# Optimization experiments

Hardware: AMD Instinct MI355X
Metric: run time of the kernel (lower is better)

Reference implementation:

```python
import jax, jax.numpy as jnp
import numpy as np

N, IN_DIM, OUT_DIM, HEADS = 8192, 256, 128, 2


def setup_inputs() -> dict:
    key = jax.random.key(0)
    k1, k2, k3, k4, k5 = jax.random.split(key, 5)
    features = jax.random.normal(k1, (N, IN_DIM), dtype=jnp.float32)
    adjacency = jax.random.randint(k2, (N, N), 0, 2, dtype=jnp.int32)
    # nn.Linear(input_dim, output_dim*heads, bias=False): weight [out, in]
    W = jax.random.normal(k3, (OUT_DIM * HEADS, IN_DIM), dtype=jnp.float32) * 0.05
    attn_src = jax.random.normal(k4, (HEADS, OUT_DIM), dtype=jnp.float32) * 0.05
    attn_dst = jax.random.normal(k5, (HEADS, OUT_DIM), dtype=jnp.float32) * 0.05
    return {"features": features, "adjacency": adjacency, "W": W,
            "attn_src": attn_src, "attn_dst": attn_dst}


def reference(features, adjacency, W, attn_src, attn_dst):
    n = features.shape[0]
    # transformed: [N, H, F]
    transformed = (features @ W.T).reshape(n, HEADS, OUT_DIM)
    src_scores = jnp.einsum('nhf,hf->nh', transformed, attn_src)  # [N, H]
    dst_scores = jnp.einsum('nhf,hf->nh', transformed, attn_dst)  # [N, H]
    # logits: [N_src, N_dst, H]
    logits = jax.nn.leaky_relu(src_scores[:, None, :] + dst_scores[None, :, :],
                               negative_slope=0.2)
    mask = adjacency > 0  # [N, N]
    logits = jnp.where(mask[:, :, None], logits, -jnp.inf)
    attention = jax.nn.softmax(logits, axis=1)  # softmax over dst dim (dim=1)
    attention = jnp.nan_to_num(attention, nan=0.0, posinf=0.0, neginf=0.0)
    aggregated = jnp.einsum('ijh,jhf->ihf', attention, transformed)  # [N, H, F]
    return aggregated.mean(axis=1)  # [N, F]
```

## Files before the change

kernel.cpp:

```cpp
#include <hip/hip_runtime.h>
#include <stdint.h>
#include <stddef.h>

#define NN 8192
#define KD 256
#define CD 256
#define FD 128
#define BI 32
#define BJ 64

typedef __attribute__((ext_vector_type(4))) float f32x4;
typedef __attribute__((ext_vector_type(8))) short b16x8;

__device__ __forceinline__ unsigned short f2bf(float x) {
    unsigned int u = __float_as_uint(x);
    u += 0x7fffu + ((u >> 16) & 1u);
    return (unsigned short)(u >> 16);
}

__device__ __forceinline__ void async16(const void* g, void* l) {
    __builtin_amdgcn_global_load_lds(
        (const __attribute__((address_space(1))) unsigned int*)g,
        (__attribute__((address_space(3))) unsigned int*)l, 16, 0, 0);
}

__global__ __launch_bounds__(256) void k_transform(
    const float* __restrict__ feat, const float* __restrict__ W,
    const float* __restrict__ asrc, const float* __restrict__ adst,
    unsigned short* __restrict__ Tt, float* __restrict__ s, float* __restrict__ d)
{
    __shared__ unsigned short a_lds[64 * 32];
    __shared__ unsigned short b_lds[256 * 32];
    __shared__ unsigned short tr_lds[256 * 72];
    __shared__ float sc_lds[4][64];
    __shared__ float dc_lds[4][64];

    const int t = threadIdx.x;
    const int wave = t >> 6, lane = t & 63;
    const int l15 = lane & 15, quad = lane >> 4;
    const int n0 = blockIdx.x * 64;
    const int ai = t >> 2, ag = t & 3;

    f32x4 acc[4][4] = {};
    for (int kc = 0; kc < 8; ++kc) {
        const int k0 = kc * 32;
        __syncthreads();
        {
            const float* src = feat + (size_t)(n0 + ai) * KD + k0 + ag * 8;
            const float4 v0 = *(const float4*)src;
            const float4 v1 = *(const float4*)(src + 4);
            union { unsigned short us[8]; b16x8 v; } pk;
            pk.us[0] = f2bf(v0.x); pk.us[1] = f2bf(v0.y);
            pk.us[2] = f2bf(v0.z); pk.us[3] = f2bf(v0.w);
            pk.us[4] = f2bf(v1.x); pk.us[5] = f2bf(v1.y);
            pk.us[6] = f2bf(v1.z); pk.us[7] = f2bf(v1.w);
            const int slot = ag ^ ((ai >> 1) & 3);
            *(b16x8*)&a_lds[ai * 32 + slot * 8] = pk.v;
        }
        for (int p = 0; p < 4; ++p) {
            const int G = p * 256 + t;
            const int c = G >> 2, g = G & 3;
            const float* src = W + (size_t)c * KD + k0 + g * 8;
            const float4 v0 = *(const float4*)src;
            const float4 v1 = *(const float4*)(src + 4);
            union { unsigned short us[8]; b16x8 v; } pk;
            pk.us[0] = f2bf(v0.x); pk.us[1] = f2bf(v0.y);
            pk.us[2] = f2bf(v0.z); pk.us[3] = f2bf(v0.w);
            pk.us[4] = f2bf(v1.x); pk.us[5] = f2bf(v1.y);
            pk.us[6] = f2bf(v1.z); pk.us[7] = f2bf(v1.w);
            const int slot = g ^ ((c >> 1) & 3);
            *(b16x8*)&b_lds[c * 32 + slot * 8] = pk.v;
        }
        __syncthreads();
        b16x8 af[4], bfr[4];
        for (int mt = 0; mt < 4; ++mt) {
            const int m = mt * 16 + l15;
            af[mt] = *(const b16x8*)&a_lds[m * 32 + (quad ^ ((m >> 1) & 3)) * 8];
        }
        for (int nt = 0; nt < 4; ++nt) {
            const int c = wave * 64 + nt * 16 + l15;
            bfr[nt] = *(const b16x8*)&b_lds[c * 32 + (quad ^ ((c >> 1) & 3)) * 8];
        }
        for (int mt = 0; mt < 4; ++mt)
            for (int nt = 0; nt < 4; ++nt)
                acc[mt][nt] = __builtin_amdgcn_mfma_f32_16x16x32_bf16(
                    af[mt], bfr[nt], acc[mt][nt], 0, 0, 0);
    }

    float aS[4], aD[4];
    for (int nt = 0; nt < 4; ++nt) {
        const int c = wave * 64 + nt * 16 + l15;
        aS[nt] = asrc[c]; aD[nt] = adst[c];
    }
    for (int mt = 0; mt < 4; ++mt)
        for (int r = 0; r < 4; ++r) {
            float vs = 0.f, vd = 0.f;
            for (int nt = 0; nt < 4; ++nt) {
                const float x = acc[mt][nt][r];
                vs += x * aS[nt]; vd += x * aD[nt];
            }
            vs += __shfl_xor(vs, 1); vd += __shfl_xor(vd, 1);
            vs += __shfl_xor(vs, 2); vd += __shfl_xor(vd, 2);
            vs += __shfl_xor(vs, 4); vd += __shfl_xor(vd, 4);
            vs += __shfl_xor(vs, 8); vd += __shfl_xor(vd, 8);
            if (l15 == 0) {
                const int nl = mt * 16 + quad * 4 + r;
                sc_lds[wave][nl] = vs; dc_lds[wave][nl] = vd;
            }
        }
    for (int mt = 0; mt < 4; ++mt)
        for (int nt = 0; nt < 4; ++nt)
            for (int r = 0; r < 4; ++r) {
                const int c = wave * 64 + nt * 16 + l15;
                const int n = mt * 16 + quad * 4 + r;
                tr_lds[c * 72 + n] = f2bf(acc[mt][nt][r]);
            }
    __syncthreads();
    if (t < 128) {
        const int n = t >> 1, h = t & 1;
        s[(size_t)(n0 + n) * 2 + h] = sc_lds[h * 2][n] + sc_lds[h * 2 + 1][n];
        d[(size_t)(n0 + n) * 2 + h] = dc_lds[h * 2][n] + dc_lds[h * 2 + 1][n];
    }
    for (int p = 0; p < 8; ++p) {
        const int idx = p * 256 + t;
        const int c = idx >> 3, g = idx & 7;
        *(b16x8*)(Tt + (size_t)c * NN + n0 + g * 8) = *(const b16x8*)&tr_lds[c * 72 + g * 8];
    }
}

__global__ __launch_bounds__(256, 4) void k_gat(
    const int* __restrict__ adj, const unsigned short* __restrict__ Tt,
    const float* __restrict__ s, const float* __restrict__ d,
    float* __restrict__ num_part,
    float* __restrict__ den_part,
    int jchunk)
{
    __shared__ unsigned short tt_lds[CD * BJ];
    __shared__ unsigned short w_lds[2 * BI * BJ];

    const int t = threadIdx.x;
    const int wave = t >> 6, lane = t & 63;
    const int l15 = lane & 15, quad = lane >> 4;
    const int i0 = blockIdx.x * BI;
    const int chunk = blockIdx.y;
    const int jbase = chunk * jchunk;

    const int wi = t >> 3;
    const int j8 = t & 7;
    const int gi = i0 + wi;
    const float s0 = s[(size_t)gi * 2 + 0];
    const float s1 = s[(size_t)gi * 2 + 1];

    const int h = wave >> 1;
    const int fh = wave & 1;
    const int cbase = h * 128 + fh * 64;

    f32x4 acc[2][4] = {};
    float den0 = 0.f, den1 = 0.f;
    const int njt = jchunk / BJ;

    for (int jt = 0; jt < njt; ++jt) {
        const int j0 = jbase + jt * BJ;
        __syncthreads();
        const int* arow = adj + (size_t)gi * NN + j0 + j8 * 8;
        const int4 a0 = *(const int4*)arow;
        const int4 a1 = *(const int4*)(arow + 4);
        const float4* dvp = (const float4*)(d + (size_t)(j0 + j8 * 8) * 2);
        union { float4 v[4]; float f[16]; } dv;
        dv.v[0] = dvp[0]; dv.v[1] = dvp[1]; dv.v[2] = dvp[2]; dv.v[3] = dvp[3];
        for (int p = 0; p < 8; ++p) {
            const int G = (p * 4 + wave) * 64 + lane;
            const int c = G >> 3, gt = G & 7;
            const int g = gt ^ (c & 7);
            async16(Tt + (size_t)c * NN + j0 + g * 8,
                    (char*)tt_lds + (size_t)(p * 4 + wave) * 1024);
        }
        const int am[8] = {a0.x, a0.y, a0.z, a0.w, a1.x, a1.y, a1.z, a1.w};
        union { unsigned short us[8]; b16x8 v; } w0, w1;
        float dp0 = 0.f, dp1 = 0.f;
        for (int e = 0; e < 8; ++e) {
            float x0 = s0 + dv.f[e * 2 + 0];  x0 = x0 > 0.f ? x0 : 0.2f * x0;
            float x1 = s1 + dv.f[e * 2 + 1];  x1 = x1 > 0.f ? x1 : 0.2f * x1;
            const float e0 = am[e] != 0 ? __expf(x0) : 0.f;
            const float e1 = am[e] != 0 ? __expf(x1) : 0.f;
            dp0 += e0; dp1 += e1;
            w0.us[e] = f2bf(e0); w1.us[e] = f2bf(e1);
        }
        den0 += dp0; den1 += dp1;
        const int slot = (j8 ^ (wi & 7)) << 3;
        *(b16x8*)&w_lds[(0 * BI + wi) * BJ + slot] = w0.v;
        *(b16x8*)&w_lds[(1 * BI + wi) * BJ + slot] = w1.v;
        __syncthreads();
        for (int ks = 0; ks < 2; ++ks) {
            const int gidx = ks * 4 + quad;
            b16x8 af[2], bfr[4];
            for (int mt = 0; mt < 2; ++mt) {
                const int m = mt * 16 + l15;
                af[mt] = *(const b16x8*)&w_lds[(h * BI + m) * BJ + ((gidx ^ (m & 7)) << 3)];
            }
            for (int nt = 0; nt < 4; ++nt) {
                const int c = cbase + nt * 16 + l15;
                bfr[nt] = *(const b16x8*)&tt_lds[c * BJ + ((gidx ^ (c & 7)) << 3)];
            }
            for (int mt = 0; mt < 2; ++mt)
                for (int nt = 0; nt < 4; ++nt)
                    acc[mt][nt] = __builtin_amdgcn_mfma_f32_16x16x32_bf16(
                        af[mt], bfr[nt], acc[mt][nt], 0, 0, 0);
        }
    }
    den0 += __shfl_xor(den0, 1); den0 += __shfl_xor(den0, 2); den0 += __shfl_xor(den0, 4);
    den1 += __shfl_xor(den1, 1); den1 += __shfl_xor(den1, 2); den1 += __shfl_xor(den1, 4);
    if (j8 == 0) {
        den_part[((size_t)chunk * 2 + 0) * NN + gi] = den0;
        den_part[((size_t)chunk * 2 + 1) * NN + gi] = den1;
    }
    float* np_ = num_part + (size_t)chunk * NN * CD;
    for (int mt = 0; mt < 2; ++mt)
        for (int nt = 0; nt < 4; ++nt)
            for (int r = 0; r < 4; ++r) {
                const int n = i0 + mt * 16 + quad * 4 + r;
                const int c = cbase + nt * 16 + l15;
                np_[(size_t)n * CD + c] = acc[mt][nt][r];
            }
}

__global__ __launch_bounds__(256) void k_combine(
    const float* __restrict__ num_part, const float* __restrict__ den_part,
    float* __restrict__ out, int jsplit)
{
    const int idx = blockIdx.x * 256 + threadIdx.x;
    const int n = idx >> 7, f = idx & 127;
    const size_t row = (size_t)n * CD;
    float n0 = 0.f, n1 = 0.f, d0 = 0.f, d1 = 0.f;
    for (int c = 0; c < jsplit; ++c) {
        const size_t base = (size_t)c * NN * CD;
        n0 += num_part[base + row + f];
        n1 += num_part[base + row + 128 + f];
        d0 += den_part[((size_t)c * 2 + 0) * NN + n];
        d1 += den_part[((size_t)c * 2 + 1) * NN + n];
    }
    const float r0 = d0 != 0.f ? n0 / d0 : 0.f;
    const float r1 = d1 != 0.f ? n1 / d1 : 0.f;
    out[idx] = 0.5f * (r0 + r1);
}

extern "C" void kernel_launch(void* const* d_in, const int* in_sizes, int n_in,
                              void* d_out, int out_size, void* d_ws, size_t ws_size,
                              hipStream_t stream) {
    const float* feat = (const float*)d_in[0];
    const int*   adj  = (const int*)d_in[1];
    const float* W    = (const float*)d_in[2];
    const float* asrc = (const float*)d_in[3];
    const float* adst = (const float*)d_in[4];
    float* out = (float*)d_out;

    const int jsplit = (ws_size >= ((size_t)40 << 20)) ? 4 : 2;
    const int jchunk = NN / jsplit;

    char* ws = (char*)d_ws;
    unsigned short* Tt = (unsigned short*)ws;
    float* s    = (float*)(ws + ((size_t)4 << 20));
    float* dsc  = (float*)(ws + ((size_t)4 << 20) + (64 << 10));
    float* den  = (float*)(ws + ((size_t)4 << 20) + (128 << 10));
    float* nump = (float*)(ws + ((size_t)8 << 20));

    k_transform<<<128, 256, 0, stream>>>(feat, W, asrc, adst, Tt, s, dsc);
    k_gat<<<dim3(NN / BI, jsplit), 256, 0, stream>>>(adj, Tt, s, dsc, nump, den, jchunk);
    k_combine<<<NN * FD / 256, 256, 0, stream>>>(nump, den, out, jsplit);
}
```

Baseline: 462.8 us.

## Load Tt fragments directly to registers, double-buffer weights, prefetch adjacency, remap blocks to XCDs

The k_gat kernel stops staging the transformed-feature tile through LDS with async global-to-LDS loads. Each wave now loads its B fragments straight from global memory into registers. The weight tile in LDS is double-buffered so only one barrier per iteration is needed. The adjacency row for the next tile is prefetched into registers. Block indices are remapped so each XCD handles one j-chunk, aiming for better L2 locality of Tt. The direct global fragment loads are less coalesced and raise register pressure, and the XCD mapping assumes gridDim.y divides 8.

```diff
diff --git a/kernel.cpp b/kernel.cpp
--- a/kernel.cpp
+++ b/kernel.cpp
@@ -16,12 +16,6 @@
     unsigned int u = __float_as_uint(x);
     u += 0x7fffu + ((u >> 16) & 1u);
     return (unsigned short)(u >> 16);
-}
-
-__device__ __forceinline__ void async16(const void* g, void* l) {
-    __builtin_amdgcn_global_load_lds(
-        (const __attribute__((address_space(1))) unsigned int*)g,
-        (__attribute__((address_space(3))) unsigned int*)l, 16, 0, 0);
 }
 
 __global__ __launch_bounds__(256) void k_transform(
@@ -135,14 +129,18 @@
     float* __restrict__ den_part,
     int jchunk)
 {
-    __shared__ unsigned short tt_lds[CD * BJ];
-    __shared__ unsigned short w_lds[2 * BI * BJ];
+    __shared__ unsigned short w_lds[2][2 * BI * BJ];
 
     const int t = threadIdx.x;
     const int wave = t >> 6, lane = t & 63;
     const int l15 = lane & 15, quad = lane >> 4;
-    const int i0 = blockIdx.x * BI;
-    const int chunk = blockIdx.y;
+
+    const int flat = blockIdx.y * gridDim.x + blockIdx.x;
+    const int xcd = flat & 7, o = flat >> 3;
+    const int xpc = 8 / gridDim.y;
+    const int chunk = xcd / xpc;
+    const int ib = (xcd % xpc) * (gridDim.x / xpc) + o;
+    const int i0 = ib * BI;
     const int jbase = chunk * jchunk;
 
     const int wi = t >> 3;
@@ -159,23 +157,23 @@
     float den0 = 0.f, den1 = 0.f;
     const int njt = jchunk / BJ;
 
+    const int* arow = adj + (size_t)gi * NN + j8 * 8;
+    int4 a0p = *(const int4*)(arow + jbase);
+    int4 a1p = *(const int4*)(arow + jbase + 4);
+
+    int buf = 0;
     for (int jt = 0; jt < njt; ++jt) {
         const int j0 = jbase + jt * BJ;
-        __syncthreads();
-        const int* arow = adj + (size_t)gi * NN + j0 + j8 * 8;
-        const int4 a0 = *(const int4*)arow;
-        const int4 a1 = *(const int4*)(arow + 4);
         const float4* dvp = (const float4*)(d + (size_t)(j0 + j8 * 8) * 2);
         union { float4 v[4]; float f[16]; } dv;
         dv.v[0] = dvp[0]; dv.v[1] = dvp[1]; dv.v[2] = dvp[2]; dv.v[3] = dvp[3];
-        for (int p = 0; p < 8; ++p) {
-            const int G = (p * 4 + wave) * 64 + lane;
-            const int c = G >> 3, gt = G & 7;
-            const int g = gt ^ (c & 7);
-            async16(Tt + (size_t)c * NN + j0 + g * 8,
-                    (char*)tt_lds + (size_t)(p * 4 + wave) * 1024);
-        }
-        const int am[8] = {a0.x, a0.y, a0.z, a0.w, a1.x, a1.y, a1.z, a1.w};
+        b16x8 bfr[2][4];
+        for (int ks = 0; ks < 2; ++ks)
+            for (int nt = 0; nt < 4; ++nt) {
+                const int c = cbase + nt * 16 + l15;
+                bfr[ks][nt] = *(const b16x8*)(Tt + (size_t)c * NN + j0 + (ks * 4 + quad) * 8);
+            }
+        const int am[8] = {a0p.x, a0p.y, a0p.z, a0p.w, a1p.x, a1p.y, a1p.z, a1p.w};
         union { unsigned short us[8]; b16x8 v; } w0, w1;
         float dp0 = 0.f, dp1 = 0.f;
         for (int e = 0; e < 8; ++e) {
@@ -188,25 +186,29 @@
         }
         den0 += dp0; den1 += dp1;
         const int slot = (j8 ^ (wi & 7)) << 3;
-        *(b16x8*)&w_lds[(0 * BI + wi) * BJ + slot] = w0.v;
-        *(b16x8*)&w_lds[(1 * BI + wi) * BJ + slot] = w1.v;
-        __syncthreads();
+        *(b16x8*)&w_lds[buf][(0 * BI + wi) * BJ + slot] = w0.v;
+        *(b16x8*)&w_lds[buf][(1 * BI + wi) * BJ + slot] = w1.v;
+        {
+            const int jn = (jt + 1 < njt) ? j0 + BJ : jbase;
+            a0p = *(const int4*)(arow + jn);
+            a1p = *(const int4*)(arow + jn + 4);
+        }
+        asm volatile("s_waitcnt lgkmcnt(0)" ::: "memory");
+        __builtin_amdgcn_s_barrier();
+        __builtin_amdgcn_sched_barrier(0);
         for (int ks = 0; ks < 2; ++ks) {
             const int gidx = ks * 4 + quad;
-            b16x8 af[2], bfr[4];
+            b16x8 af[2];
             for (int mt = 0; mt < 2; ++mt) {
                 const int m = mt * 16 + l15;
-                af[mt] = *(const b16x8*)&w_lds[(h * BI + m) * BJ + ((gidx ^ (m & 7)) << 3)];
-            }
-            for (int nt = 0; nt < 4; ++nt) {
-                const int c = cbase + nt * 16 + l15;
-                bfr[nt] = *(const b16x8*)&tt_lds[c * BJ + ((gidx ^ (c & 7)) << 3)];
+                af[mt] = *(const b16x8*)&w_lds[buf][(h * BI + m) * BJ + ((gidx ^ (m & 7)) << 3)];
             }
             for (int mt = 0; mt < 2; ++mt)
                 for (int nt = 0; nt < 4; ++nt)
                     acc[mt][nt] = __builtin_amdgcn_mfma_f32_16x16x32_bf16(
-                        af[mt], bfr[nt], acc[mt][nt], 0, 0, 0);
-        }
+                        af[mt], bfr[ks][nt], acc[mt][nt], 0, 0, 0);
+        }
+        buf ^= 1;
     }
     den0 += __shfl_xor(den0, 1); den0 += __shfl_xor(den0, 2); den0 += __shfl_xor(den0, 4);
     den1 += __shfl_xor(den1, 1); den1 += __shfl_xor(den1, 2); den1 += __shfl_xor(den1, 4);
```

After: 498.7 us. 7.7% more time.

## Double row tile to 64 with 512 threads, prefetch adjacency, allow 8-way j split

Applied to the files above, without the earlier changes.

Raises the k_gat row tile from 32 to 64 rows and uses 512 threads (8 waves), so each staged Tt tile in LDS is reused by twice as many rows and global Tt traffic is halved. It also prefetches the next adjacency row slice one iteration ahead, to hide global load latency behind the exp/softmax weight computation. When the workspace is large enough, the j dimension is split 8 ways to keep the halved grid filling the device. The costs are more LDS and register pressure per block, lower occupancy, and larger partial-sum buffers for the combine kernel to read.

```diff
diff --git a/kernel.cpp b/kernel.cpp
--- a/kernel.cpp
+++ b/kernel.cpp
@@ -6,7 +6,7 @@
 #define KD 256
 #define CD 256
 #define FD 128
-#define BI 32
+#define BI 64
 #define BJ 64
 
 typedef __attribute__((ext_vector_type(4))) float f32x4;
@@ -128,7 +128,7 @@
     }
 }
 
-__global__ __launch_bounds__(256, 4) void k_gat(
+__global__ __launch_bounds__(512, 4) void k_gat(
     const int* __restrict__ adj, const unsigned short* __restrict__ Tt,
     const float* __restrict__ s, const float* __restrict__ d,
     float* __restrict__ num_part,
@@ -139,8 +139,11 @@
     __shared__ unsigned short w_lds[2 * BI * BJ];
 
     const int t = threadIdx.x;
-    const int wave = t >> 6, lane = t & 63;
+    const int w = t >> 6, lane = t & 63;
     const int l15 = lane & 15, quad = lane >> 4;
+    const int h  = (w >> 2) & 1;
+    const int fh = (w >> 1) & 1;
+    const int rh = w & 1;
     const int i0 = blockIdx.x * BI;
     const int chunk = blockIdx.y;
     const int jbase = chunk * jchunk;
@@ -150,32 +153,33 @@
     const int gi = i0 + wi;
     const float s0 = s[(size_t)gi * 2 + 0];
     const float s1 = s[(size_t)gi * 2 + 1];
-
-    const int h = wave >> 1;
-    const int fh = wave & 1;
     const int cbase = h * 128 + fh * 64;
 
     f32x4 acc[2][4] = {};
     float den0 = 0.f, den1 = 0.f;
     const int njt = jchunk / BJ;
 
+    const int* arow = adj + (size_t)gi * NN + j8 * 8;
+    int4 a0p = *(const int4*)(arow + jbase);
+    int4 a1p = *(const int4*)(arow + jbase + 4);
+
     for (int jt = 0; jt < njt; ++jt) {
         const int j0 = jbase + jt * BJ;
         __syncthreads();
-        const int* arow = adj + (size_t)gi * NN + j0 + j8 * 8;
-        const int4 a0 = *(const int4*)arow;
-        const int4 a1 = *(const int4*)(arow + 4);
         const float4* dvp = (const float4*)(d + (size_t)(j0 + j8 * 8) * 2);
         union { float4 v[4]; float f[16]; } dv;
         dv.v[0] = dvp[0]; dv.v[1] = dvp[1]; dv.v[2] = dvp[2]; dv.v[3] = dvp[3];
-        for (int p = 0; p < 8; ++p) {
-            const int G = (p * 4 + wave) * 64 + lane;
+        for (int p = 0; p < 4; ++p) {
+            const int G = (p * 8 + w) * 64 + lane;
             const int c = G >> 3, gt = G & 7;
             const int g = gt ^ (c & 7);
             async16(Tt + (size_t)c * NN + j0 + g * 8,
-                    (char*)tt_lds + (size_t)(p * 4 + wave) * 1024);
-        }
-        const int am[8] = {a0.x, a0.y, a0.z, a0.w, a1.x, a1.y, a1.z, a1.w};
+                    (char*)tt_lds + (size_t)(p * 8 + w) * 1024);
+        }
+        const int jn = (jt + 1 < njt) ? j0 + BJ : jbase;
+        const int4 aN0 = *(const int4*)(arow + jn);
+        const int4 aN1 = *(const int4*)(arow + jn + 4);
+        const int am[8] = {a0p.x, a0p.y, a0p.z, a0p.w, a1p.x, a1p.y, a1p.z, a1p.w};
         union { unsigned short us[8]; b16x8 v; } w0, w1;
         float dp0 = 0.f, dp1 = 0.f;
         for (int e = 0; e < 8; ++e) {
@@ -190,12 +194,13 @@
         const int slot = (j8 ^ (wi & 7)) << 3;
         *(b16x8*)&w_lds[(0 * BI + wi) * BJ + slot] = w0.v;
         *(b16x8*)&w_lds[(1 * BI + wi) * BJ + slot] = w1.v;
+        a0p = aN0; a1p = aN1;
         __syncthreads();
         for (int ks = 0; ks < 2; ++ks) {
             const int gidx = ks * 4 + quad;
             b16x8 af[2], bfr[4];
             for (int mt = 0; mt < 2; ++mt) {
-                const int m = mt * 16 + l15;
+                const int m = rh * 32 + mt * 16 + l15;
                 af[mt] = *(const b16x8*)&w_lds[(h * BI + m) * BJ + ((gidx ^ (m & 7)) << 3)];
             }
             for (int nt = 0; nt < 4; ++nt) {
@@ -218,7 +223,7 @@
     for (int mt = 0; mt < 2; ++mt)
         for (int nt = 0; nt < 4; ++nt)
             for (int r = 0; r < 4; ++r) {
-                const int n = i0 + mt * 16 + quad * 4 + r;
+                const int n = i0 + rh * 32 + mt * 16 + quad * 4 + r;
                 const int c = cbase + nt * 16 + l15;
                 np_[(size_t)n * CD + c] = acc[mt][nt][r];
             }
@@ -254,7 +259,8 @@
     const float* adst = (const float*)d_in[4];
     float* out = (float*)d_out;
 
-    const int jsplit = (ws_size >= ((size_t)40 << 20)) ? 4 : 2;
+    const int jsplit = (ws_size >= ((size_t)73 << 20)) ? 8
+                     : (ws_size >= ((size_t)40 << 20)) ? 4 : 2;
     const int jchunk = NN / jsplit;
 
     char* ws = (char*)d_ws;
@@ -265,6 +271,6 @@
     float* nump = (float*)(ws + ((size_t)8 << 20));
 
     k_transform<<<128, 256, 0, stream>>>(feat, W, asrc, adst, Tt, s, dsc);
-    k_gat<<<dim3(NN / BI, jsplit), 256, 0, stream>>>(adj, Tt, s, dsc, nump, den, jchunk);
+    k_gat<<<dim3(NN / BI, jsplit), 512, 0, stream>>>(adj, Tt, s, dsc, nump, den, jchunk);
     k_combine<<<NN * FD / 256, 256, 0, stream>>>(nump, den, out, jsplit);
 }
```

Result: slower. 477.6 us (+3.2%).
